# Kernel optimization log

Measured on AMD Instinct MI355X. Metric: run time of the kernel, lower is better.

Reference implementation:

```python
import jax, jax.numpy as jnp
import numpy as np

DT = 0.1  # fixed Euler base step, as in the torch module
B, D, H = 65536, 64, 128


def setup_inputs() -> dict:
    key = jax.random.key(0)
    ks = jax.random.split(key, 9)
    z = jax.random.normal(ks[0], (B, D), dtype=jnp.float32)
    # time_delta in [-2, 2) -> steps = ceil(max|td|/0.1) ~= 20
    time_delta = jax.random.uniform(ks[1], (B,), dtype=jnp.float32, minval=-2.0, maxval=2.0)

    def lin_init(kw, kb, fan_in, fan_out):
        bound = 1.0 / np.sqrt(fan_in)
        W = jax.random.uniform(kw, (fan_in, fan_out), jnp.float32, -bound, bound)
        b = jax.random.uniform(kb, (fan_out,), jnp.float32, -bound, bound)
        return W, b

    W1, b1 = lin_init(ks[2], ks[3], D + 1, H)
    W2, b2 = lin_init(ks[4], ks[5], H, H)
    W3, b3 = lin_init(ks[6], ks[7], H, D)
    return dict(z=z, time_delta=time_delta, W1=W1, b1=b1, W2=W2, b2=b2, W3=W3, b3=b3)


def reference(z, time_delta, W1, b1, W2, b2, W3, b3):
    # steps is derived from concrete input data (as in the torch .item() call)
    steps = int(np.ceil(float(jnp.max(jnp.abs(time_delta))) / DT))
    if steps == 0:
        return z
    actual_dt = (time_delta / steps)[:, None]          # [B, 1]
    ts = jnp.arange(steps, dtype=z.dtype) * DT         # time feature per step (scalar, batch-uniform)

    Wz, Wt = W1[:-1], W1[-1]  # concat([z, t*ones]) @ W1 == z @ Wz + t * Wt

    def step(z_c, t):
        h = jnp.tanh(z_c @ Wz + t * Wt + b1)           # [B, H]
        h = jnp.tanh(h @ W2 + b2)                      # [B, H]
        dz = h @ W3 + b3                               # [B, D]
        return z_c + dz * actual_dt, None

    z_final, _ = jax.lax.scan(step, z, ts)
    return z_final
```

## Files before the change

### kernel.cpp

```cpp
#include <hip/hip_runtime.h>

#define B_N 65536
#define D_N 64
#define H_N 128
#define K_SCALE 2.885390081777927f

typedef __attribute__((ext_vector_type(8))) __bf16 bf16x8;
typedef __attribute__((ext_vector_type(8))) unsigned short ushort8;
typedef __attribute__((ext_vector_type(4))) float f32x4;
typedef __attribute__((ext_vector_type(4))) unsigned int uint32x4;


__device__ __forceinline__ unsigned short f2bf(float f) {
    unsigned u = __float_as_uint(f);
    u += 0x7FFFu + ((u >> 16) & 1u);
    return (unsigned short)(u >> 16);
}

__device__ __forceinline__ float tanh_scaled(float a) {
    float e;
    asm("v_exp_f32 %0, %1" : "=v"(e) : "v"(a));
    return fmaf(-2.0f, __builtin_amdgcn_rcpf(e + 1.0f), 1.0f);
}

__device__ __forceinline__ unsigned cvt_pk_bf16(float lo, float hi) {
    unsigned r;
    asm("v_cvt_pk_bf16_f32 %0, %1, %2" : "=v"(r) : "v"(lo), "v"(hi));
    return r;
}

__device__ __forceinline__ int sigma(int m) {
    return (m & 96) | ((m & 4) << 2) | ((m >> 1) & 12) | (m & 3);
}

__global__ void k_pre(const float* __restrict__ td, const float* __restrict__ W1,
                      const float* __restrict__ W2, const float* __restrict__ W3,
                      unsigned* __restrict__ ws) {
    if (blockIdx.x < 64) {
        int i = blockIdx.x * blockDim.x + threadIdx.x;
        float m = 0.0f;
        for (; i < B_N; i += 64 * 256) m = fmaxf(m, fabsf(td[i]));
#pragma unroll
        for (int o = 32; o; o >>= 1) m = fmaxf(m, __shfl_down(m, o));
        if ((threadIdx.x & 63) == 0) atomicMax(ws, __float_as_uint(m));
    } else {
        int i = (blockIdx.x - 64) * 256 + threadIdx.x;
        unsigned short* wsb = (unsigned short*)(ws + 16);
        float v;
        if (i < 8192) {
            int n = i >> 6, m = i & 63;
            v = W1[sigma(m) * 128 + n] * K_SCALE;
        } else if (i < 24576) {
            int o = i - 8192;
            int n = o >> 7, m = o & 127;
            v = W2[sigma(m) * 128 + n] * K_SCALE;
        } else {
            int o = i - 24576;
            int n = o >> 7, m = o & 127;
            v = W3[sigma(m) * 64 + n];
        }
        wsb[i] = f2bf(v);
    }
}

__launch_bounds__(256, 1)
__global__ void k_main(const float* __restrict__ z_in, const float* __restrict__ td,
                       const float* __restrict__ W1, const float* __restrict__ b1,
                       const float* __restrict__ b2, const float* __restrict__ b3,
                       const void* __restrict__ ws, float* __restrict__ out) {
    const unsigned* wsu = (const unsigned*)ws;
    const unsigned short* wzg = (const unsigned short*)((const char*)ws + 64);
    const unsigned short* w2g = wzg + 8192;
    const unsigned short* w3g = wzg + 24576;

    const int tid = threadIdx.x;
    const int wave = tid >> 6;
    const int lane = tid & 63;
    const int q = lane >> 4;
    const int m15 = lane & 15;

    bf16x8 wzf[8][2];
    bf16x8 w2f[8][4];
    bf16x8 w3f[4][4];
    bf16x8 augf[8];
#pragma unroll
    for (int n0 = 0; n0 < 8; ++n0)
#pragma unroll
        for (int kt = 0; kt < 2; ++kt)
            wzf[n0][kt] = __builtin_bit_cast(
                bf16x8, *(const ushort8*)&wzg[(n0 * 16 + m15) * 64 + kt * 32 + q * 8]);
#pragma unroll
    for (int n0 = 0; n0 < 8; ++n0)
#pragma unroll
        for (int kt = 0; kt < 4; ++kt)
            w2f[n0][kt] = __builtin_bit_cast(
                bf16x8, *(const ushort8*)&w2g[(n0 * 16 + m15) * 128 + kt * 32 + q * 8]);
#pragma unroll
    for (int n0 = 0; n0 < 4; ++n0)
#pragma unroll
        for (int kt = 0; kt < 4; ++kt)
            w3f[n0][kt] = __builtin_bit_cast(
                bf16x8, *(const ushort8*)&w3g[(n0 * 16 + m15) * 128 + kt * 32 + q * 8]);
#pragma unroll
    for (int n0 = 0; n0 < 8; ++n0) {
        const int n = n0 * 16 + m15;
        float wt = W1[64 * 128 + n] * K_SCALE;
        float bb = b1[n] * K_SCALE;
        unsigned w = (unsigned)f2bf(wt) | ((unsigned)f2bf(bb) << 16);
        w = (q == 0) ? w : 0u;
        augf[n0] = __builtin_bit_cast(bf16x8, (uint32x4){w, 0u, 0u, 0u});
    }

    f32x4 b2c[8];
#pragma unroll
    for (int n0 = 0; n0 < 8; ++n0) {
        f32x4 v = *(const f32x4*)&b2[n0 * 16 + q * 4];
#pragma unroll
        for (int r = 0; r < 4; ++r) v[r] *= K_SCALE;
        b2c[n0] = v;
    }

    const float maxab = __uint_as_float(wsu[0]);
    const int steps = (int)ceil((double)maxab / 0.1);

    for (int tile = 0; tile < 4; ++tile) {
        const int row = blockIdx.x * 256 + tile * 64 + wave * 16 + m15;

        float zr[16];
#pragma unroll
        for (int kt = 0; kt < 2; ++kt)
#pragma unroll
            for (int hi = 0; hi < 2; ++hi) {
                f32x4 v = *(const f32x4*)(z_in + (size_t)row * 64 + kt * 32 + hi * 16 + q * 4);
#pragma unroll
                for (int r = 0; r < 4; ++r) zr[kt * 8 + hi * 4 + r] = v[r];
            }
        const float tdr = td[row];
        const float dtr = (steps > 0) ? (tdr / (float)steps) : 0.0f;

        for (int s = 0; s < steps; ++s) {
            const float t = (float)s * 0.1f;

            unsigned za[8];
#pragma unroll
            for (int i = 0; i < 8; ++i) za[i] = cvt_pk_bf16(zr[2 * i], zr[2 * i + 1]);
            unsigned tw = cvt_pk_bf16(t, 1.0f);
            tw = (q == 0) ? tw : 0u;
            bf16x8 zA0 = __builtin_bit_cast(bf16x8, (uint32x4){za[0], za[1], za[2], za[3]});
            bf16x8 zA1 = __builtin_bit_cast(bf16x8, (uint32x4){za[4], za[5], za[6], za[7]});
            bf16x8 zA2 = __builtin_bit_cast(bf16x8, (uint32x4){tw, 0u, 0u, 0u});

            unsigned hv[16];
#pragma unroll
            for (int n0 = 0; n0 < 8; ++n0) {
                f32x4 acc = {0.f, 0.f, 0.f, 0.f};
                acc = __builtin_amdgcn_mfma_f32_16x16x32_bf16(wzf[n0][0], zA0, acc, 0, 0, 0);
                acc = __builtin_amdgcn_mfma_f32_16x16x32_bf16(wzf[n0][1], zA1, acc, 0, 0, 0);
                acc = __builtin_amdgcn_mfma_f32_16x16x32_bf16(augf[n0],   zA2, acc, 0, 0, 0);
                hv[n0 * 2 + 0] = cvt_pk_bf16(tanh_scaled(acc[0]), tanh_scaled(acc[1]));
                hv[n0 * 2 + 1] = cvt_pk_bf16(tanh_scaled(acc[2]), tanh_scaled(acc[3]));
            }

            unsigned gv[16];
#pragma unroll
            for (int n0 = 0; n0 < 8; ++n0) {
                f32x4 acc = b2c[n0];
#pragma unroll
                for (int kt = 0; kt < 4; ++kt) {
                    bf16x8 hf = __builtin_bit_cast(
                        bf16x8, (uint32x4){hv[4 * kt], hv[4 * kt + 1],
                                           hv[4 * kt + 2], hv[4 * kt + 3]});
                    acc = __builtin_amdgcn_mfma_f32_16x16x32_bf16(w2f[n0][kt], hf, acc, 0, 0, 0);
                }
                gv[n0 * 2 + 0] = cvt_pk_bf16(tanh_scaled(acc[0]), tanh_scaled(acc[1]));
                gv[n0 * 2 + 1] = cvt_pk_bf16(tanh_scaled(acc[2]), tanh_scaled(acc[3]));
            }

#pragma unroll
            for (int n0 = 0; n0 < 4; ++n0) {
                f32x4 acc = {0.f, 0.f, 0.f, 0.f};
#pragma unroll
                for (int kt = 0; kt < 4; ++kt) {
                    bf16x8 gf = __builtin_bit_cast(
                        bf16x8, (uint32x4){gv[4 * kt], gv[4 * kt + 1],
                                           gv[4 * kt + 2], gv[4 * kt + 3]});
                    acc = __builtin_amdgcn_mfma_f32_16x16x32_bf16(w3f[n0][kt], gf, acc, 0, 0, 0);
                }
#pragma unroll
                for (int r = 0; r < 4; ++r)
                    zr[n0 * 4 + r] = fmaf(acc[r], dtr, zr[n0 * 4 + r]);
            }
        }

        const float tb3 = (steps > 0) ? tdr : 0.0f;
#pragma unroll
        for (int n0 = 0; n0 < 4; ++n0) {
            f32x4 bb = *(const f32x4*)&b3[n0 * 16 + q * 4];
#pragma unroll
            for (int r = 0; r < 4; ++r)
                zr[n0 * 4 + r] = fmaf(tb3, bb[r], zr[n0 * 4 + r]);
        }

#pragma unroll
        for (int kt = 0; kt < 2; ++kt)
#pragma unroll
            for (int hi = 0; hi < 2; ++hi) {
                f32x4 v;
#pragma unroll
                for (int r = 0; r < 4; ++r) v[r] = zr[kt * 8 + hi * 4 + r];
                *(f32x4*)(out + (size_t)row * 64 + kt * 32 + hi * 16 + q * 4) = v;
            }
    }
}

extern "C" void kernel_launch(void* const* d_in, const int* in_sizes, int n_in,
                              void* d_out, int out_size, void* d_ws, size_t ws_size,
                              hipStream_t stream) {
    const float* z  = (const float*)d_in[0];
    const float* td = (const float*)d_in[1];
    const float* W1 = (const float*)d_in[2];
    const float* b1 = (const float*)d_in[3];
    const float* W2 = (const float*)d_in[4];
    const float* b2 = (const float*)d_in[5];
    const float* W3 = (const float*)d_in[6];
    const float* b3 = (const float*)d_in[7];
    float* out = (float*)d_out;
    (void)in_sizes; (void)n_in; (void)out_size; (void)ws_size;

    hipMemsetAsync(d_ws, 0, 64, stream);
    k_pre<<<192, 256, 0, stream>>>(td, W1, W2, W3, (unsigned*)d_ws);
    k_main<<<256, 256, 0, stream>>>(z, td, W1, b1, b2, b3, d_ws, out);
}
```

Baseline: 208.5 us.

## Fuse preprocessing into single kernel and interleave two row tiles per wave

Removes the memset and weight-preprocessing kernel: each block now reduces max|td| itself and builds bf16 weight fragments from fp32 weights staged in shared memory. The step loop processes two independent 16-row tiles per wave together, giving the scheduler independent MFMA and tanh chains to overlap latency. Costs include every block re-reading the full td array and a large LDS footprint, plus higher register pressure from doubled state.

```diff
diff --git a/kernel.cpp b/kernel.cpp
--- a/kernel.cpp
+++ b/kernel.cpp
@@ -1,21 +1,11 @@
 #include <hip/hip_runtime.h>
 
 #define B_N 65536
-#define D_N 64
-#define H_N 128
 #define K_SCALE 2.885390081777927f
 
 typedef __attribute__((ext_vector_type(8))) __bf16 bf16x8;
-typedef __attribute__((ext_vector_type(8))) unsigned short ushort8;
 typedef __attribute__((ext_vector_type(4))) float f32x4;
 typedef __attribute__((ext_vector_type(4))) unsigned int uint32x4;
-
-
-__device__ __forceinline__ unsigned short f2bf(float f) {
-    unsigned u = __float_as_uint(f);
-    u += 0x7FFFu + ((u >> 16) & 1u);
-    return (unsigned short)(u >> 16);
-}
 
 __device__ __forceinline__ float tanh_scaled(float a) {
     float e;
@@ -33,51 +23,52 @@
     return (m & 96) | ((m & 4) << 2) | ((m >> 1) & 12) | (m & 3);
 }
 
-__global__ void k_pre(const float* __restrict__ td, const float* __restrict__ W1,
-                      const float* __restrict__ W2, const float* __restrict__ W3,
-                      unsigned* __restrict__ ws) {
-    if (blockIdx.x < 64) {
-        int i = blockIdx.x * blockDim.x + threadIdx.x;
-        float m = 0.0f;
-        for (; i < B_N; i += 64 * 256) m = fmaxf(m, fabsf(td[i]));
-#pragma unroll
-        for (int o = 32; o; o >>= 1) m = fmaxf(m, __shfl_down(m, o));
-        if ((threadIdx.x & 63) == 0) atomicMax(ws, __float_as_uint(m));
-    } else {
-        int i = (blockIdx.x - 64) * 256 + threadIdx.x;
-        unsigned short* wsb = (unsigned short*)(ws + 16);
-        float v;
-        if (i < 8192) {
-            int n = i >> 6, m = i & 63;
-            v = W1[sigma(m) * 128 + n] * K_SCALE;
-        } else if (i < 24576) {
-            int o = i - 8192;
-            int n = o >> 7, m = o & 127;
-            v = W2[sigma(m) * 128 + n] * K_SCALE;
-        } else {
-            int o = i - 24576;
-            int n = o >> 7, m = o & 127;
-            v = W3[sigma(m) * 64 + n];
-        }
-        wsb[i] = f2bf(v);
-    }
-}
-
 __launch_bounds__(256, 1)
-__global__ void k_main(const float* __restrict__ z_in, const float* __restrict__ td,
-                       const float* __restrict__ W1, const float* __restrict__ b1,
-                       const float* __restrict__ b2, const float* __restrict__ b3,
-                       const void* __restrict__ ws, float* __restrict__ out) {
-    const unsigned* wsu = (const unsigned*)ws;
-    const unsigned short* wzg = (const unsigned short*)((const char*)ws + 64);
-    const unsigned short* w2g = wzg + 8192;
-    const unsigned short* w3g = wzg + 24576;
+__global__ void k_all(const float* __restrict__ z_in, const float* __restrict__ td,
+                      const float* __restrict__ W1, const float* __restrict__ b1,
+                      const float* __restrict__ W2, const float* __restrict__ b2,
+                      const float* __restrict__ W3, const float* __restrict__ b3,
+                      float* __restrict__ out) {
+    __shared__ float w1s[65 * 128];
+    __shared__ float w2s[128 * 128];
+    __shared__ float w3s[128 * 64];
+    __shared__ float red[4];
 
     const int tid = threadIdx.x;
-    const int wave = tid >> 6;
-    const int lane = tid & 63;
-    const int q = lane >> 4;
-    const int m15 = lane & 15;
+    const int wave = tid >> 6, lane = tid & 63;
+    const int q = lane >> 4, m15 = lane & 15;
+
+    float mx = 0.0f;
+    const f32x4* tdv = (const f32x4*)td;
+    for (int c = tid; c < B_N / 4; c += 256) {
+        f32x4 v = tdv[c];
+        mx = fmaxf(mx, fmaxf(fmaxf(fabsf(v[0]), fabsf(v[1])),
+                             fmaxf(fabsf(v[2]), fabsf(v[3]))));
+    }
+#pragma unroll
+    for (int o = 32; o; o >>= 1) mx = fmaxf(mx, __shfl_down(mx, o));
+    if (lane == 0) red[wave] = mx;
+
+    for (int c = tid; c < 2080; c += 256) ((f32x4*)w1s)[c] = ((const f32x4*)W1)[c];
+    for (int c = tid; c < 4096; c += 256) ((f32x4*)w2s)[c] = ((const f32x4*)W2)[c];
+    for (int c = tid; c < 2048; c += 256) ((f32x4*)w3s)[c] = ((const f32x4*)W3)[c];
+    __syncthreads();
+
+    const float maxab = fmaxf(fmaxf(red[0], red[1]), fmaxf(red[2], red[3]));
+    const int steps = (int)ceil((double)maxab / 0.1);
+
+    const int col128 = m15;
+    auto mkfrag = [&](const float* base, int ldn, int col, int mbase,
+                      float scale) -> bf16x8 {
+        unsigned w[4];
+#pragma unroll
+        for (int jp = 0; jp < 4; ++jp) {
+            float lo = base[sigma(mbase + 2 * jp) * ldn + col] * scale;
+            float hi = base[sigma(mbase + 2 * jp + 1) * ldn + col] * scale;
+            w[jp] = cvt_pk_bf16(lo, hi);
+        }
+        return __builtin_bit_cast(bf16x8, (uint32x4){w[0], w[1], w[2], w[3]});
+    };
 
     bf16x8 wzf[8][2];
     bf16x8 w2f[8][4];
@@ -87,26 +78,21 @@
     for (int n0 = 0; n0 < 8; ++n0)
 #pragma unroll
         for (int kt = 0; kt < 2; ++kt)
-            wzf[n0][kt] = __builtin_bit_cast(
-                bf16x8, *(const ushort8*)&wzg[(n0 * 16 + m15) * 64 + kt * 32 + q * 8]);
+            wzf[n0][kt] = mkfrag(w1s, 128, n0 * 16 + col128, kt * 32 + q * 8, K_SCALE);
 #pragma unroll
     for (int n0 = 0; n0 < 8; ++n0)
 #pragma unroll
         for (int kt = 0; kt < 4; ++kt)
-            w2f[n0][kt] = __builtin_bit_cast(
-                bf16x8, *(const ushort8*)&w2g[(n0 * 16 + m15) * 128 + kt * 32 + q * 8]);
+            w2f[n0][kt] = mkfrag(w2s, 128, n0 * 16 + col128, kt * 32 + q * 8, K_SCALE);
 #pragma unroll
     for (int n0 = 0; n0 < 4; ++n0)
 #pragma unroll
         for (int kt = 0; kt < 4; ++kt)
-            w3f[n0][kt] = __builtin_bit_cast(
-                bf16x8, *(const ushort8*)&w3g[(n0 * 16 + m15) * 128 + kt * 32 + q * 8]);
+            w3f[n0][kt] = mkfrag(w3s, 64, n0 * 16 + col128, kt * 32 + q * 8, 1.0f);
 #pragma unroll
     for (int n0 = 0; n0 < 8; ++n0) {
         const int n = n0 * 16 + m15;
-        float wt = W1[64 * 128 + n] * K_SCALE;
-        float bb = b1[n] * K_SCALE;
-        unsigned w = (unsigned)f2bf(wt) | ((unsigned)f2bf(bb) << 16);
+        unsigned w = cvt_pk_bf16(w1s[64 * 128 + n] * K_SCALE, b1[n] * K_SCALE);
         w = (q == 0) ? w : 0u;
         augf[n0] = __builtin_bit_cast(bf16x8, (uint32x4){w, 0u, 0u, 0u});
     }
@@ -120,96 +106,108 @@
         b2c[n0] = v;
     }
 
-    const float maxab = __uint_as_float(wsu[0]);
-    const int steps = (int)ceil((double)maxab / 0.1);
-
-    for (int tile = 0; tile < 4; ++tile) {
-        const int row = blockIdx.x * 256 + tile * 64 + wave * 16 + m15;
-
-        float zr[16];
-#pragma unroll
-        for (int kt = 0; kt < 2; ++kt)
-#pragma unroll
-            for (int hi = 0; hi < 2; ++hi) {
-                f32x4 v = *(const f32x4*)(z_in + (size_t)row * 64 + kt * 32 + hi * 16 + q * 4);
-#pragma unroll
-                for (int r = 0; r < 4; ++r) zr[kt * 8 + hi * 4 + r] = v[r];
+    for (int p = 0; p < 2; ++p) {
+        const int row0 = blockIdx.x * 256 + (2 * p) * 64 + wave * 16 + m15;
+
+        float zr[2][16];
+        float dtr[2], tdr[2];
+#pragma unroll
+        for (int u = 0; u < 2; ++u) {
+            const int row = row0 + u * 64;
+#pragma unroll
+            for (int kt = 0; kt < 2; ++kt)
+#pragma unroll
+                for (int hi = 0; hi < 2; ++hi) {
+                    f32x4 v = *(const f32x4*)(z_in + (size_t)row * 64 + kt * 32 + hi * 16 + q * 4);
+#pragma unroll
+                    for (int r = 0; r < 4; ++r) zr[u][kt * 8 + hi * 4 + r] = v[r];
+                }
+            tdr[u] = td[row];
+            dtr[u] = (steps > 0) ? (tdr[u] / (float)steps) : 0.0f;
+        }
+
+        for (int s = 0; s < steps; ++s) {
+            const float tt = (float)s * 0.1f;
+            unsigned tws = cvt_pk_bf16(tt, 1.0f);
+            tws = (q == 0) ? tws : 0u;
+            const bf16x8 zA2 = __builtin_bit_cast(bf16x8, (uint32x4){tws, 0u, 0u, 0u});
+
+            unsigned hv[2][16];
+#pragma unroll
+            for (int u = 0; u < 2; ++u) {
+                unsigned za[8];
+#pragma unroll
+                for (int i = 0; i < 8; ++i)
+                    za[i] = cvt_pk_bf16(zr[u][2 * i], zr[u][2 * i + 1]);
+                const bf16x8 zA0 = __builtin_bit_cast(bf16x8, (uint32x4){za[0], za[1], za[2], za[3]});
+                const bf16x8 zA1 = __builtin_bit_cast(bf16x8, (uint32x4){za[4], za[5], za[6], za[7]});
+#pragma unroll
+                for (int n0 = 0; n0 < 8; ++n0) {
+                    f32x4 acc = {0.f, 0.f, 0.f, 0.f};
+                    acc = __builtin_amdgcn_mfma_f32_16x16x32_bf16(wzf[n0][0], zA0, acc, 0, 0, 0);
+                    acc = __builtin_amdgcn_mfma_f32_16x16x32_bf16(wzf[n0][1], zA1, acc, 0, 0, 0);
+                    acc = __builtin_amdgcn_mfma_f32_16x16x32_bf16(augf[n0],   zA2, acc, 0, 0, 0);
+                    hv[u][n0 * 2 + 0] = cvt_pk_bf16(tanh_scaled(acc[0]), tanh_scaled(acc[1]));
+                    hv[u][n0 * 2 + 1] = cvt_pk_bf16(tanh_scaled(acc[2]), tanh_scaled(acc[3]));
+                }
             }
-        const float tdr = td[row];
-        const float dtr = (steps > 0) ? (tdr / (float)steps) : 0.0f;
-
-        for (int s = 0; s < steps; ++s) {
-            const float t = (float)s * 0.1f;
-
-            unsigned za[8];
-#pragma unroll
-            for (int i = 0; i < 8; ++i) za[i] = cvt_pk_bf16(zr[2 * i], zr[2 * i + 1]);
-            unsigned tw = cvt_pk_bf16(t, 1.0f);
-            tw = (q == 0) ? tw : 0u;
-            bf16x8 zA0 = __builtin_bit_cast(bf16x8, (uint32x4){za[0], za[1], za[2], za[3]});
-            bf16x8 zA1 = __builtin_bit_cast(bf16x8, (uint32x4){za[4], za[5], za[6], za[7]});
-            bf16x8 zA2 = __builtin_bit_cast(bf16x8, (uint32x4){tw, 0u, 0u, 0u});
-
-            unsigned hv[16];
-#pragma unroll
-            for (int n0 = 0; n0 < 8; ++n0) {
-                f32x4 acc = {0.f, 0.f, 0.f, 0.f};
-                acc = __builtin_amdgcn_mfma_f32_16x16x32_bf16(wzf[n0][0], zA0, acc, 0, 0, 0);
-                acc = __builtin_amdgcn_mfma_f32_16x16x32_bf16(wzf[n0][1], zA1, acc, 0, 0, 0);
-                acc = __builtin_amdgcn_mfma_f32_16x16x32_bf16(augf[n0],   zA2, acc, 0, 0, 0);
-                hv[n0 * 2 + 0] = cvt_pk_bf16(tanh_scaled(acc[0]), tanh_scaled(acc[1]));
-                hv[n0 * 2 + 1] = cvt_pk_bf16(tanh_scaled(acc[2]), tanh_scaled(acc[3]));
+
+            unsigned gv[2][16];
+#pragma unroll
+            for (int u = 0; u < 2; ++u)
+#pragma unroll
+                for (int n0 = 0; n0 < 8; ++n0) {
+                    f32x4 acc = b2c[n0];
+#pragma unroll
+                    for (int kt = 0; kt < 4; ++kt) {
+                        const bf16x8 hf = __builtin_bit_cast(
+                            bf16x8, (uint32x4){hv[u][4 * kt], hv[u][4 * kt + 1],
+                                               hv[u][4 * kt + 2], hv[u][4 * kt + 3]});
+                        acc = __builtin_amdgcn_mfma_f32_16x16x32_bf16(w2f[n0][kt], hf, acc, 0, 0, 0);
+                    }
+                    gv[u][n0 * 2 + 0] = cvt_pk_bf16(tanh_scaled(acc[0]), tanh_scaled(acc[1]));
+                    gv[u][n0 * 2 + 1] = cvt_pk_bf16(tanh_scaled(acc[2]), tanh_scaled(acc[3]));
+                }
+
+#pragma unroll
+            for (int u = 0; u < 2; ++u)
+#pragma unroll
+                for (int n0 = 0; n0 < 4; ++n0) {
+                    f32x4 acc = {0.f, 0.f, 0.f, 0.f};
+#pragma unroll
+                    for (int kt = 0; kt < 4; ++kt) {
+                        const bf16x8 gf = __builtin_bit_cast(
+                            bf16x8, (uint32x4){gv[u][4 * kt], gv[u][4 * kt + 1],
+                                               gv[u][4 * kt + 2], gv[u][4 * kt + 3]});
+                        acc = __builtin_amdgcn_mfma_f32_16x16x32_bf16(w3f[n0][kt], gf, acc, 0, 0, 0);
+                    }
+#pragma unroll
+                    for (int r = 0; r < 4; ++r)
+                        zr[u][n0 * 4 + r] = fmaf(acc[r], dtr[u], zr[u][n0 * 4 + r]);
+                }
+        }
+
+#pragma unroll
+        for (int u = 0; u < 2; ++u) {
+            const int row = row0 + u * 64;
+            const float tb3 = (steps > 0) ? tdr[u] : 0.0f;
+#pragma unroll
+            for (int n0 = 0; n0 < 4; ++n0) {
+                f32x4 bb = *(const f32x4*)&b3[n0 * 16 + q * 4];
+#pragma unroll
+                for (int r = 0; r < 4; ++r)
+                    zr[u][n0 * 4 + r] = fmaf(tb3, bb[r], zr[u][n0 * 4 + r]);
             }
-
-            unsigned gv[16];
-#pragma unroll
-            for (int n0 = 0; n0 < 8; ++n0) {
-                f32x4 acc = b2c[n0];
-#pragma unroll
-                for (int kt = 0; kt < 4; ++kt) {
-                    bf16x8 hf = __builtin_bit_cast(
-                        bf16x8, (uint32x4){hv[4 * kt], hv[4 * kt + 1],
-                                           hv[4 * kt + 2], hv[4 * kt + 3]});
-                    acc = __builtin_amdgcn_mfma_f32_16x16x32_bf16(w2f[n0][kt], hf, acc, 0, 0, 0);
-                }
-                gv[n0 * 2 + 0] = cvt_pk_bf16(tanh_scaled(acc[0]), tanh_scaled(acc[1]));
-                gv[n0 * 2 + 1] = cvt_pk_bf16(tanh_scaled(acc[2]), tanh_scaled(acc[3]));
-            }
-
-#pragma unroll
-            for (int n0 = 0; n0 < 4; ++n0) {
-                f32x4 acc = {0.f, 0.f, 0.f, 0.f};
-#pragma unroll
-                for (int kt = 0; kt < 4; ++kt) {
-                    bf16x8 gf = __builtin_bit_cast(
-                        bf16x8, (uint32x4){gv[4 * kt], gv[4 * kt + 1],
-                                           gv[4 * kt + 2], gv[4 * kt + 3]});
-                    acc = __builtin_amdgcn_mfma_f32_16x16x32_bf16(w3f[n0][kt], gf, acc, 0, 0, 0);
-                }
-#pragma unroll
-                for (int r = 0; r < 4; ++r)
-                    zr[n0 * 4 + r] = fmaf(acc[r], dtr, zr[n0 * 4 + r]);
-            }
-        }
-
-        const float tb3 = (steps > 0) ? tdr : 0.0f;
-#pragma unroll
-        for (int n0 = 0; n0 < 4; ++n0) {
-            f32x4 bb = *(const f32x4*)&b3[n0 * 16 + q * 4];
-#pragma unroll
-            for (int r = 0; r < 4; ++r)
-                zr[n0 * 4 + r] = fmaf(tb3, bb[r], zr[n0 * 4 + r]);
-        }
-
-#pragma unroll
-        for (int kt = 0; kt < 2; ++kt)
-#pragma unroll
-            for (int hi = 0; hi < 2; ++hi) {
-                f32x4 v;
-#pragma unroll
-                for (int r = 0; r < 4; ++r) v[r] = zr[kt * 8 + hi * 4 + r];
-                *(f32x4*)(out + (size_t)row * 64 + kt * 32 + hi * 16 + q * 4) = v;
-            }
+#pragma unroll
+            for (int kt = 0; kt < 2; ++kt)
+#pragma unroll
+                for (int hi = 0; hi < 2; ++hi) {
+                    f32x4 v;
+#pragma unroll
+                    for (int r = 0; r < 4; ++r) v[r] = zr[u][kt * 8 + hi * 4 + r];
+                    *(f32x4*)(out + (size_t)row * 64 + kt * 32 + hi * 16 + q * 4) = v;
+                }
+        }
     }
 }
 
@@ -225,9 +223,7 @@
     const float* W3 = (const float*)d_in[6];
     const float* b3 = (const float*)d_in[7];
     float* out = (float*)d_out;
-    (void)in_sizes; (void)n_in; (void)out_size; (void)ws_size;
-
-    hipMemsetAsync(d_ws, 0, 64, stream);
-    k_pre<<<192, 256, 0, stream>>>(td, W1, W2, W3, (unsigned*)d_ws);
-    k_main<<<256, 256, 0, stream>>>(z, td, W1, b1, b2, b3, d_ws, out);
-}
+    (void)in_sizes; (void)n_in; (void)out_size; (void)d_ws; (void)ws_size;
+
+    k_all<<<256, 256, 0, stream>>>(z, td, W1, b1, W2, b2, W3, b3, out);
+}
```

Result: slower. 229.5 us (+10.1%).
